# Performance work log

Measured on AMD Instinct MI355X. Metric: run time of the kernel, lower is better.

The kernel has to match this reference:

```python
import jax, jax.numpy as jnp
import numpy as np

CLASS_COUNT = 21
THRESHOLD = 0.5
ALPHA = 0.25
GAMMA = 2.0
VARIANCE = (0.1, 0.2)

B, A, N_OBJ = 32, 24576, 16


def point_form(boxes):
    # center form (cx, cy, w, h) -> point form (xmin, ymin, xmax, ymax)
    return jnp.concatenate([boxes[:, :2] - boxes[:, 2:] / 2,
                            boxes[:, :2] + boxes[:, 2:] / 2], axis=1)


def jaccard(truths, priors):
    # truths [N,4], priors [A,4] both in point form -> IoU [N, A]
    lt = jnp.maximum(truths[:, None, :2], priors[None, :, :2])
    rb = jnp.minimum(truths[:, None, 2:], priors[None, :, 2:])
    wh = jnp.clip(rb - lt, 0.0, None)
    inter = wh[..., 0] * wh[..., 1]
    area_t = ((truths[:, 2] - truths[:, 0]) * (truths[:, 3] - truths[:, 1]))[:, None]
    area_p = ((priors[:, 2] - priors[:, 0]) * (priors[:, 3] - priors[:, 1]))[None, :]
    return inter / (area_t + area_p - inter)


def match_one(labels, truths, anchors):
    # labels [N] int, truths [N,4] point form, anchors [A,4] center form
    overlaps = jaccard(truths, point_form(anchors))           # [N, A]
    best_prior_idx = jnp.argmax(overlaps, axis=1)             # [N]
    best_truth_overlap = jnp.max(overlaps, axis=0)            # [A]
    best_truth_idx = jnp.argmax(overlaps, axis=0)             # [A]
    # ensure every gt matches its best prior
    best_truth_overlap = best_truth_overlap.at[best_prior_idx].set(2.0)
    best_truth_idx = best_truth_idx.at[best_prior_idx].set(jnp.arange(truths.shape[0]))
    matches = truths[best_truth_idx]                          # [A, 4]
    conf = jnp.where(best_truth_overlap < THRESHOLD, 0, labels[best_truth_idx])
    # encode with variances
    g_cxcy = ((matches[:, :2] + matches[:, 2:]) * 0.5 - anchors[:, :2]) / (VARIANCE[0] * anchors[:, 2:])
    g_wh = jnp.log((matches[:, 2:] - matches[:, :2]) / anchors[:, 2:]) / VARIANCE[1]
    return conf, jnp.concatenate([g_cxcy, g_wh], axis=1)


def setup_inputs() -> dict:
    key = jax.random.key(0)
    k1, k2, k3, k4, k5, k6, k7 = jax.random.split(key, 7)
    class_preds = jax.random.normal(k1, (B, A, CLASS_COUNT), dtype=jnp.float32)
    loc_preds = jax.random.normal(k2, (B, A, 4), dtype=jnp.float32)
    # ground-truth boxes: random valid point-form boxes in [0,1]
    ctr = jax.random.uniform(k3, (B, N_OBJ, 2), minval=0.2, maxval=0.8)
    wh = jax.random.uniform(k4, (B, N_OBJ, 2), minval=0.05, maxval=0.3)
    loc_targets = jnp.clip(jnp.concatenate([ctr - wh / 2, ctr + wh / 2], axis=-1), 0.0, 1.0)
    class_targets = jax.random.randint(k5, (B, N_OBJ), 1, CLASS_COUNT)
    # anchors in center form
    a_ctr = jax.random.uniform(k6, (A, 2), minval=0.05, maxval=0.95)
    a_wh = jax.random.uniform(k7, (A, 2), minval=0.05, maxval=0.4)
    anchors = jnp.concatenate([a_ctr, a_wh], axis=1)
    return {"class_preds": class_preds, "loc_preds": loc_preds,
            "loc_targets": loc_targets, "anchors": anchors,
            "class_targets": class_targets}


def reference(class_preds, loc_preds, loc_targets, anchors, class_targets):
    conf, loc_t = jax.vmap(match_one, in_axes=(0, 0, None))(class_targets, loc_targets, anchors)
    pos = conf > 0                                            # [B, A]
    num_matched = jnp.sum(pos).astype(jnp.float32)
    # smooth L1 over positive anchors (sum reduction, beta=1)
    d = loc_preds - loc_t
    ad = jnp.abs(d)
    sl1 = jnp.where(ad < 1.0, 0.5 * d * d, ad - 0.5)
    loc_loss = jnp.sum(sl1 * pos[..., None].astype(sl1.dtype))
    # focal loss (drop background column 0)
    cp = class_preds.reshape(-1, CLASS_COUNT)[:, 1:]          # [B*A, C-1]
    t = jax.nn.one_hot(conf.reshape(-1), CLASS_COUNT, dtype=cp.dtype)[:, 1:]
    p = jax.nn.sigmoid(cp)
    pt = jnp.where(t > 0, p, 1.0 - p)
    w = (1.0 - pt) ** GAMMA
    w = jnp.where(t > 0, ALPHA * w, (1.0 - ALPHA) * w)
    # stable binary cross entropy with logits, weighted, sum reduction
    bce = jnp.maximum(cp, 0.0) - cp * t + jnp.log1p(jnp.exp(-jnp.abs(cp)))
    class_loss = jnp.sum(w * bce)
    class_loss = class_loss / num_matched
    loc_loss = loc_loss / num_matched
    return jnp.stack([class_loss, loc_loss, class_loss + loc_loss])
```

## Files before the change

### kernel.cpp

```cpp
#include <hip/hip_runtime.h>

#define A_COUNT 24576
#define B_COUNT 32
#define NOBJ 16
#define C_COUNT 21

#define NCH 64
#define CHUNK (A_COUNT / NCH)
#define NBLK (NCH * B_COUNT)
#define TOTAL4 (B_COUNT * A_COUNT * C_COUNT / 4)

#define WS_BPP 0
#define WS_LOCP 262144
#define WS_CLSP 270336
#define WS_POSP 278528
#define WS_DLOC 286720
#define WS_DCLS 286848
#define WS_DPOS 286976

__device__ __forceinline__ unsigned long long pack_key(float iou, int a) {
    unsigned int ib = __float_as_uint(iou);
    return ((unsigned long long)ib << 32) | (unsigned long long)(0xFFFFFFFFu - (unsigned int)a);
}

__device__ __forceinline__ float iou_pf(float tx0, float ty0, float tx1, float ty1, float at,
                                        float x0, float y0, float x1, float y1, float ap) {
    float lx = fmaxf(tx0, x0), ly = fmaxf(ty0, y0);
    float rx = fminf(tx1, x1), ry = fminf(ty1, y1);
    float w = fmaxf(rx - lx, 0.0f), h = fmaxf(ry - ly, 0.0f);
    float inter = w * h;
    return inter / (at + ap - inter);
}

__device__ __forceinline__ float sl1(float d) {
    float ad = fabsf(d);
    return (ad < 1.0f) ? 0.5f * d * d : ad - 0.5f;
}

__device__ __forceinline__ float loc_term(float4 t, float4 an, float4 lp) {
    float gx = ((t.x + t.z) * 0.5f - an.x) / (0.1f * an.z);
    float gy = ((t.y + t.w) * 0.5f - an.y) / (0.1f * an.w);
    float gw = __logf((t.z - t.x) / an.z) * 5.0f;
    float gh = __logf((t.w - t.y) / an.w) * 5.0f;
    return sl1(lp.x - gx) + sl1(lp.y - gy) + sl1(lp.z - gw) + sl1(lp.w - gh);
}

__device__ __forceinline__ float corr_term(float x) {
    float E = __expf(x);
    float den = 1.0f + E;
    float s = __builtin_amdgcn_rcpf(den);
    float p = E * s;
    float L = __logf(den);
    return 0.25f * s * s * (L - x) - 0.75f * p * p * L;
}

__global__ __launch_bounds__(256, 2) void k_main(const float* __restrict__ cls,
                                                 const float4* __restrict__ locp,
                                                 const float4* __restrict__ anchors,
                                                 const float4* __restrict__ truths,
                                                 const int* __restrict__ labels,
                                                 unsigned long long* __restrict__ bp_partial,
                                                 float* __restrict__ loc_partial,
                                                 float* __restrict__ cls_partial,
                                                 unsigned int* __restrict__ pos_partial) {
    const int ch = blockIdx.x;
    const int b = blockIdx.y;
    const int tid = threadIdx.x;
    __shared__ float4 s_t[NOBJ];
    __shared__ float s_area[NOBJ];
    __shared__ int s_lab[NOBJ];
    __shared__ unsigned long long s_keys[8][256];
    if (tid < NOBJ) {
        float4 t = truths[b * NOBJ + tid];
        s_t[tid] = t;
        s_area[tid] = (t.z - t.x) * (t.w - t.y);
        s_lab[tid] = labels[b * NOBJ + tid];
    }
    __syncthreads();
    const int a0 = ch * CHUNK + tid;
    const bool has1 = tid < (CHUNK - 256);
    const int a1 = a0 + 256;
    float4 an0 = anchors[a0];
    float4 an1 = anchors[has1 ? a1 : a0];
    float p0x0 = an0.x - an0.z * 0.5f, p0y0 = an0.y - an0.w * 0.5f;
    float p0x1 = an0.x + an0.z * 0.5f, p0y1 = an0.y + an0.w * 0.5f;
    float ap0 = (p0x1 - p0x0) * (p0y1 - p0y0);
    float p1x0 = an1.x - an1.z * 0.5f, p1y0 = an1.y - an1.w * 0.5f;
    float p1x1 = an1.x + an1.z * 0.5f, p1y1 = an1.y + an1.w * 0.5f;
    float ap1 = (p1x1 - p1x0) * (p1y1 - p1y0);
    float best0 = -1.0f, best1 = -1.0f;
    int idx0 = 0, idx1 = 0;
#pragma unroll
    for (int half = 0; half < 2; ++half) {
#pragma unroll
        for (int n = 0; n < 8; ++n) {
            const int nt = half * 8 + n;
            float4 t = s_t[nt];
            float at = s_area[nt];
            float iou0 = iou_pf(t.x, t.y, t.z, t.w, at, p0x0, p0y0, p0x1, p0y1, ap0);
            if (iou0 > best0) { best0 = iou0; idx0 = nt; }
            unsigned long long key = pack_key(iou0, a0);
            if (has1) {
                float iou1 = iou_pf(t.x, t.y, t.z, t.w, at, p1x0, p1y0, p1x1, p1y1, ap1);
                if (iou1 > best1) { best1 = iou1; idx1 = nt; }
                unsigned long long k1 = pack_key(iou1, a1);
                key = (k1 > key) ? k1 : key;
            }
            s_keys[n][tid] = key;
        }
        __syncthreads();
        if (tid < 128) {
            const int g = tid >> 4, l = tid & 15;
            unsigned long long k = s_keys[g][l];
#pragma unroll
            for (int kk = 1; kk < 16; ++kk) {
                unsigned long long v = s_keys[g][l + 16 * kk];
                k = (v > k) ? v : k;
            }
#pragma unroll
            for (int s = 8; s >= 1; s >>= 1) {
                unsigned long long o = __shfl_xor(k, s);
                k = (o > k) ? o : k;
            }
            if (l == 0) bp_partial[(b * NOBJ + half * 8 + g) * NCH + ch] = k;
        }
        __syncthreads();
    }
    float loc_l = 0.0f, cls_acc = 0.0f;
    unsigned int pos = 0;
    if (!(best0 < 0.5f)) {
        pos++;
        loc_l += loc_term(s_t[idx0], an0, locp[(size_t)b * A_COUNT + a0]);
        cls_acc += corr_term(cls[((size_t)b * A_COUNT + a0) * C_COUNT + s_lab[idx0]]);
    }
    if (has1 && !(best1 < 0.5f)) {
        pos++;
        loc_l += loc_term(s_t[idx1], an1, locp[(size_t)b * A_COUNT + a1]);
        cls_acc += corr_term(cls[((size_t)b * A_COUNT + a1) * C_COUNT + s_lab[idx1]]);
    }

    const int bid = b * NCH + ch;
    {
        const float4* cls4 = (const float4*)cls;
        int i = bid * 256 + tid;
        unsigned int f = (unsigned int)i * 4u;
        unsigned int dq = f / 21u;
        int r = (int)(f - dq * 21u);
        const int stride = NBLK * 256;
        for (; i < TOTAL4; i += stride) {
            float4 x4 = cls4[i];
            float xs[4] = {x4.x, x4.y, x4.z, x4.w};
#pragma unroll
            for (int j = 0; j < 4; ++j) {
                int rr = r + j;
                float x = xs[j];
                float E = __expf(x);
                float den = 1.0f + E;
                float s = __builtin_amdgcn_rcpf(den);
                float p = E * s;
                float L = __logf(den);
                float v = p * p * L;
                float m = (rr == 0 || rr == 21) ? 0.0f : 0.75f;
                cls_acc = fmaf(v, m, cls_acc);
            }
            r += 8; if (r >= 21) r -= 21;
        }
    }

#pragma unroll
    for (int s = 32; s >= 1; s >>= 1) {
        loc_l += __shfl_xor(loc_l, s);
        cls_acc += __shfl_xor(cls_acc, s);
        pos += __shfl_xor(pos, s);
    }
    __shared__ float s_ll[4], s_cl[4];
    __shared__ unsigned int s_pp[4];
    if ((tid & 63) == 0) {
        s_ll[tid >> 6] = loc_l;
        s_cl[tid >> 6] = cls_acc;
        s_pp[tid >> 6] = pos;
    }
    __syncthreads();
    if (tid == 0) {
        loc_partial[bid] = s_ll[0] + s_ll[1] + s_ll[2] + s_ll[3];
        cls_partial[bid] = s_cl[0] + s_cl[1] + s_cl[2] + s_cl[3];
        pos_partial[bid] = s_pp[0] + s_pp[1] + s_pp[2] + s_pp[3];
    }
}

__global__ __launch_bounds__(256) void k_fix(const float* __restrict__ cls,
                                             const float4* __restrict__ locp,
                                             const float4* __restrict__ anchors,
                                             const float4* __restrict__ truths,
                                             const int* __restrict__ labels,
                                             const unsigned long long* __restrict__ bp_partial,
                                             float* __restrict__ dloc,
                                             float* __restrict__ dcls,
                                             int* __restrict__ dpos) {
    const int b = blockIdx.x;
    const int tid = threadIdx.x;
    __shared__ int s_bp[NOBJ];
    {
        const int g = tid >> 4, l = tid & 15;
        const unsigned long long* pp = &bp_partial[(size_t)(b * NOBJ + g) * NCH];
        unsigned long long k = pp[l];
        unsigned long long v;
        v = pp[l + 16]; k = (v > k) ? v : k;
        v = pp[l + 32]; k = (v > k) ? v : k;
        v = pp[l + 48]; k = (v > k) ? v : k;
#pragma unroll
        for (int s = 8; s >= 1; s >>= 1) {
            unsigned long long o = __shfl_xor(k, s);
            k = (o > k) ? o : k;
        }
        if (l == 0) {
            unsigned int ia = 0xFFFFFFFFu - (unsigned int)(k & 0xFFFFFFFFull);
            s_bp[g] = (ia >= A_COUNT) ? -1 : (int)ia;
        }
    }
    __syncthreads();
    float d_loc = 0.0f, d_cls = 0.0f;
    int d_pos = 0;
    if (tid < NOBJ) {
        const int n = tid;
        const int q = s_bp[n];
        bool winner = (q >= 0);
        for (int n2 = n + 1; n2 < NOBJ; ++n2)
            if (s_bp[n2] == q) winner = false;
        if (winner) {
            float4 an = anchors[q];
            float px0 = an.x - an.z * 0.5f, py0 = an.y - an.w * 0.5f;
            float px1 = an.x + an.z * 0.5f, py1 = an.y + an.w * 0.5f;
            float ap = (px1 - px0) * (py1 - py0);
            float best = -1.0f;
            int idx = 0;
            for (int n2 = 0; n2 < NOBJ; ++n2) {
                float4 t = truths[b * NOBJ + n2];
                float at = (t.z - t.x) * (t.w - t.y);
                float iou = iou_pf(t.x, t.y, t.z, t.w, at, px0, py0, px1, py1, ap);
                if (iou > best) { best = iou; idx = n2; }
            }
            float4 lp = locp[(size_t)b * A_COUNT + q];
            if (!(best < 0.5f)) {
                d_pos -= 1;
                d_loc -= loc_term(truths[b * NOBJ + idx], an, lp);
                d_cls -= corr_term(cls[((size_t)b * A_COUNT + q) * C_COUNT + labels[b * NOBJ + idx]]);
            }
            d_pos += 1;
            d_loc += loc_term(truths[b * NOBJ + n], an, lp);
            d_cls += corr_term(cls[((size_t)b * A_COUNT + q) * C_COUNT + labels[b * NOBJ + n]]);
        }
    }
    if (tid < 64) {
#pragma unroll
        for (int s = 8; s >= 1; s >>= 1) {
            d_loc += __shfl_xor(d_loc, s);
            d_cls += __shfl_xor(d_cls, s);
            d_pos += __shfl_xor(d_pos, s);
        }
        if (tid == 0) {
            dloc[b] = d_loc;
            dcls[b] = d_cls;
            dpos[b] = d_pos;
        }
    }
}

__global__ __launch_bounds__(256) void k_final(const float* __restrict__ loc_partial,
                                               const float* __restrict__ cls_partial,
                                               const unsigned int* __restrict__ pos_partial,
                                               const float* __restrict__ dloc,
                                               const float* __restrict__ dcls,
                                               const int* __restrict__ dpos,
                                               float* __restrict__ out) {
    const int tid = threadIdx.x;
    double loc = 0.0, clsv = 0.0;
    int pos = 0;
    for (int i = tid; i < NBLK; i += 256) {
        loc += (double)loc_partial[i];
        clsv += (double)cls_partial[i];
        pos += (int)pos_partial[i];
    }
    if (tid < B_COUNT) {
        loc += (double)dloc[tid];
        clsv += (double)dcls[tid];
        pos += dpos[tid];
    }
#pragma unroll
    for (int s = 32; s >= 1; s >>= 1) {
        loc += __shfl_xor(loc, s);
        clsv += __shfl_xor(clsv, s);
        pos += __shfl_xor(pos, s);
    }
    __shared__ double s_l[4], s_c[4];
    __shared__ int s_p[4];
    if ((tid & 63) == 0) {
        s_l[tid >> 6] = loc;
        s_c[tid >> 6] = clsv;
        s_p[tid >> 6] = pos;
    }
    __syncthreads();
    if (tid == 0) {
        double L = s_l[0] + s_l[1] + s_l[2] + s_l[3];
        double Cv = s_c[0] + s_c[1] + s_c[2] + s_c[3];
        float nm = (float)(s_p[0] + s_p[1] + s_p[2] + s_p[3]);
        float cf = (float)Cv / nm;
        float lf = (float)L / nm;
        out[0] = cf;
        out[1] = lf;
        out[2] = cf + lf;
    }
}

extern "C" void kernel_launch(void* const* d_in, const int* in_sizes, int n_in,
                              void* d_out, int out_size, void* d_ws, size_t ws_size,
                              hipStream_t stream) {
    const float* cls = (const float*)d_in[0];
    const float4* locp = (const float4*)d_in[1];
    const float4* truths = (const float4*)d_in[2];
    const float4* anchors = (const float4*)d_in[3];
    const int* labels = (const int*)d_in[4];

    char* ws = (char*)d_ws;
    unsigned long long* bp_partial = (unsigned long long*)(ws + WS_BPP);
    float* loc_partial = (float*)(ws + WS_LOCP);
    float* cls_partial = (float*)(ws + WS_CLSP);
    unsigned int* pos_partial = (unsigned int*)(ws + WS_POSP);
    float* dloc = (float*)(ws + WS_DLOC);
    float* dcls = (float*)(ws + WS_DCLS);
    int* dpos = (int*)(ws + WS_DPOS);

    k_main<<<dim3(NCH, B_COUNT), 256, 0, stream>>>(cls, locp, anchors, truths, labels,
                                                   bp_partial, loc_partial, cls_partial, pos_partial);
    k_fix<<<B_COUNT, 256, 0, stream>>>(cls, locp, anchors, truths, labels, bp_partial,
                                       dloc, dcls, dpos);
    k_final<<<1, 256, 0, stream>>>(loc_partial, cls_partial, pos_partial, dloc, dcls, dpos,
                                   (float*)d_out);
}
```

Before: 42.99 us.

## Prefetch class-logit stream into registers before IoU matching to overlap loads

Issues all eight strided float4 loads of class logits per thread up front, before the IoU/argmax matching phase, so global memory latency overlaps with matching compute. The grid-stride loop becomes a fully unrolled fixed 8-iteration loop with four independent accumulators. Occupancy hint rises from 2 to 4 blocks per SM, and __syncthreads is replaced by an LDS-only waitcnt plus raw barrier so barriers do not wait on the outstanding global prefetches. This raises register pressure (32 extra VGPRs held across the matching phase) and hardcodes the iteration count to the problem size.

```diff
diff --git a/kernel.cpp b/kernel.cpp
--- a/kernel.cpp
+++ b/kernel.cpp
@@ -9,6 +9,7 @@
 #define CHUNK (A_COUNT / NCH)
 #define NBLK (NCH * B_COUNT)
 #define TOTAL4 (B_COUNT * A_COUNT * C_COUNT / 4)
+#define STRIDE4 (NBLK * 256)
 
 #define WS_BPP 0
 #define WS_LOCP 262144
@@ -54,7 +55,16 @@
     return 0.25f * s * s * (L - x) - 0.75f * p * p * L;
 }
 
-__global__ __launch_bounds__(256, 2) void k_main(const float* __restrict__ cls,
+#define FOC(xval, rr, acc) {                                 \
+    float E_ = __expf(xval);                                 \
+    float den_ = 1.0f + E_;                                  \
+    float s_ = __builtin_amdgcn_rcpf(den_);                  \
+    float p_ = E_ * s_;                                      \
+    float L_ = __logf(den_);                                 \
+    float m_ = ((rr) == 0 || (rr) == 21) ? 0.0f : 0.75f;     \
+    acc = fmaf(p_ * p_ * L_, m_, acc); }
+
+__global__ __launch_bounds__(256, 4) void k_main(const float* __restrict__ cls,
                                                  const float4* __restrict__ locp,
                                                  const float4* __restrict__ anchors,
                                                  const float4* __restrict__ truths,
@@ -77,11 +87,27 @@
         s_lab[tid] = labels[b * NOBJ + tid];
     }
     __syncthreads();
+    __builtin_amdgcn_sched_barrier(0);
+
     const int a0 = ch * CHUNK + tid;
     const bool has1 = tid < (CHUNK - 256);
     const int a1 = a0 + 256;
     float4 an0 = anchors[a0];
     float4 an1 = anchors[has1 ? a1 : a0];
+
+    const int bid = b * NCH + ch;
+    const float4* cls4 = (const float4*)cls;
+    const int i0 = bid * 256 + tid;
+    const bool v7 = (i0 + 7 * STRIDE4) < TOTAL4;
+    float4 xv[8];
+#pragma unroll
+    for (int k = 0; k < 8; ++k) {
+        const int ik = i0 + k * STRIDE4;
+        if (k < 7) xv[k] = cls4[ik];
+        else       xv[7] = v7 ? cls4[ik] : make_float4(0.f, 0.f, 0.f, 0.f);
+    }
+    __builtin_amdgcn_sched_barrier(0);
+
     float p0x0 = an0.x - an0.z * 0.5f, p0y0 = an0.y - an0.w * 0.5f;
     float p0x1 = an0.x + an0.z * 0.5f, p0y1 = an0.y + an0.w * 0.5f;
     float ap0 = (p0x1 - p0x0) * (p0y1 - p0y0);
@@ -108,7 +134,8 @@
             }
             s_keys[n][tid] = key;
         }
-        __syncthreads();
+        asm volatile("s_waitcnt lgkmcnt(0)" ::: "memory");
+        __builtin_amdgcn_s_barrier();
         if (tid < 128) {
             const int g = tid >> 4, l = tid & 15;
             unsigned long long k = s_keys[g][l];
@@ -124,7 +151,8 @@
             }
             if (l == 0) bp_partial[(b * NOBJ + half * 8 + g) * NCH + ch] = k;
         }
-        __syncthreads();
+        asm volatile("s_waitcnt lgkmcnt(0)" ::: "memory");
+        __builtin_amdgcn_s_barrier();
     }
     float loc_l = 0.0f, cls_acc = 0.0f;
     unsigned int pos = 0;
@@ -139,32 +167,21 @@
         cls_acc += corr_term(cls[((size_t)b * A_COUNT + a1) * C_COUNT + s_lab[idx1]]);
     }
 
-    const int bid = b * NCH + ch;
     {
-        const float4* cls4 = (const float4*)cls;
-        int i = bid * 256 + tid;
-        unsigned int f = (unsigned int)i * 4u;
+        unsigned int f = (unsigned int)i0 * 4u;
         unsigned int dq = f / 21u;
         int r = (int)(f - dq * 21u);
-        const int stride = NBLK * 256;
-        for (; i < TOTAL4; i += stride) {
-            float4 x4 = cls4[i];
-            float xs[4] = {x4.x, x4.y, x4.z, x4.w};
-#pragma unroll
-            for (int j = 0; j < 4; ++j) {
-                int rr = r + j;
-                float x = xs[j];
-                float E = __expf(x);
-                float den = 1.0f + E;
-                float s = __builtin_amdgcn_rcpf(den);
-                float p = E * s;
-                float L = __logf(den);
-                float v = p * p * L;
-                float m = (rr == 0 || rr == 21) ? 0.0f : 0.75f;
-                cls_acc = fmaf(v, m, cls_acc);
+        float acc0 = 0.0f, acc1 = 0.0f, acc2 = 0.0f, acc3 = 0.0f;
+#pragma unroll
+        for (int k = 0; k < 8; ++k) {
+            if (k < 7 || v7) {
+                float4 x4 = xv[k];
+                FOC(x4.x, r + 0, acc0); FOC(x4.y, r + 1, acc1);
+                FOC(x4.z, r + 2, acc2); FOC(x4.w, r + 3, acc3);
             }
             r += 8; if (r >= 21) r -= 21;
         }
+        cls_acc += (acc0 + acc1) + (acc2 + acc3);
     }
 
 #pragma unroll
```

After: 46.89 us. 1.09x slower.

## Split anchors into 96 chunks with one anchor per thread and split accumulators

Applied to the files above, without the earlier changes.

Raises the anchor chunk count from 64 to 96 so each 256-thread block handles exactly 256 anchors, one per thread, removing the second-anchor path. Workspace offsets, the streaming stride and the fix-kernel partial reduction are updated to match, and launch bounds now ask for 4 blocks per SM. The focal streaming loop uses four independent accumulators with the 0.75 factor applied once at the end, and IoU division becomes a hardware reciprocal. This adds more blocks and more partials to reduce, trading per-thread work for occupancy and ILP. The approximate reciprocal may slightly change argmax tie behaviour.

```diff
diff --git a/kernel.cpp b/kernel.cpp
--- a/kernel.cpp
+++ b/kernel.cpp
@@ -5,18 +5,19 @@
 #define NOBJ 16
 #define C_COUNT 21
 
-#define NCH 64
+#define NCH 96
 #define CHUNK (A_COUNT / NCH)
 #define NBLK (NCH * B_COUNT)
 #define TOTAL4 (B_COUNT * A_COUNT * C_COUNT / 4)
+#define STRIDE4 (NBLK * 256)
 
 #define WS_BPP 0
-#define WS_LOCP 262144
-#define WS_CLSP 270336
-#define WS_POSP 278528
-#define WS_DLOC 286720
-#define WS_DCLS 286848
-#define WS_DPOS 286976
+#define WS_LOCP 393216
+#define WS_CLSP 405504
+#define WS_POSP 417792
+#define WS_DLOC 430080
+#define WS_DCLS 430208
+#define WS_DPOS 430336
 
 __device__ __forceinline__ unsigned long long pack_key(float iou, int a) {
     unsigned int ib = __float_as_uint(iou);
@@ -29,7 +30,7 @@
     float rx = fminf(tx1, x1), ry = fminf(ty1, y1);
     float w = fmaxf(rx - lx, 0.0f), h = fmaxf(ry - ly, 0.0f);
     float inter = w * h;
-    return inter / (at + ap - inter);
+    return inter * __builtin_amdgcn_rcpf(at + ap - inter);
 }
 
 __device__ __forceinline__ float sl1(float d) {
@@ -54,7 +55,16 @@
     return 0.25f * s * s * (L - x) - 0.75f * p * p * L;
 }
 
-__global__ __launch_bounds__(256, 2) void k_main(const float* __restrict__ cls,
+#define FOC(xval, rr, acc) {                                 \
+    float E_ = __expf(xval);                                 \
+    float den_ = 1.0f + E_;                                  \
+    float s_ = __builtin_amdgcn_rcpf(den_);                  \
+    float p_ = E_ * s_;                                      \
+    float L_ = __logf(den_);                                 \
+    float v_ = ((rr) == 0 || (rr) == 21) ? 0.0f : p_ * p_ * L_; \
+    acc += v_; }
+
+__global__ __launch_bounds__(256, 4) void k_main(const float* __restrict__ cls,
                                                  const float4* __restrict__ locp,
                                                  const float4* __restrict__ anchors,
                                                  const float4* __restrict__ truths,
@@ -78,18 +88,12 @@
     }
     __syncthreads();
     const int a0 = ch * CHUNK + tid;
-    const bool has1 = tid < (CHUNK - 256);
-    const int a1 = a0 + 256;
     float4 an0 = anchors[a0];
-    float4 an1 = anchors[has1 ? a1 : a0];
     float p0x0 = an0.x - an0.z * 0.5f, p0y0 = an0.y - an0.w * 0.5f;
     float p0x1 = an0.x + an0.z * 0.5f, p0y1 = an0.y + an0.w * 0.5f;
     float ap0 = (p0x1 - p0x0) * (p0y1 - p0y0);
-    float p1x0 = an1.x - an1.z * 0.5f, p1y0 = an1.y - an1.w * 0.5f;
-    float p1x1 = an1.x + an1.z * 0.5f, p1y1 = an1.y + an1.w * 0.5f;
-    float ap1 = (p1x1 - p1x0) * (p1y1 - p1y0);
-    float best0 = -1.0f, best1 = -1.0f;
-    int idx0 = 0, idx1 = 0;
+    float best0 = -1.0f;
+    int idx0 = 0;
 #pragma unroll
     for (int half = 0; half < 2; ++half) {
 #pragma unroll
@@ -99,14 +103,7 @@
             float at = s_area[nt];
             float iou0 = iou_pf(t.x, t.y, t.z, t.w, at, p0x0, p0y0, p0x1, p0y1, ap0);
             if (iou0 > best0) { best0 = iou0; idx0 = nt; }
-            unsigned long long key = pack_key(iou0, a0);
-            if (has1) {
-                float iou1 = iou_pf(t.x, t.y, t.z, t.w, at, p1x0, p1y0, p1x1, p1y1, ap1);
-                if (iou1 > best1) { best1 = iou1; idx1 = nt; }
-                unsigned long long k1 = pack_key(iou1, a1);
-                key = (k1 > key) ? k1 : key;
-            }
-            s_keys[n][tid] = key;
+            s_keys[n][tid] = pack_key(iou0, a0);
         }
         __syncthreads();
         if (tid < 128) {
@@ -126,45 +123,30 @@
         }
         __syncthreads();
     }
-    float loc_l = 0.0f, cls_acc = 0.0f;
+    float loc_l = 0.0f, corr_acc = 0.0f;
     unsigned int pos = 0;
     if (!(best0 < 0.5f)) {
-        pos++;
-        loc_l += loc_term(s_t[idx0], an0, locp[(size_t)b * A_COUNT + a0]);
-        cls_acc += corr_term(cls[((size_t)b * A_COUNT + a0) * C_COUNT + s_lab[idx0]]);
-    }
-    if (has1 && !(best1 < 0.5f)) {
-        pos++;
-        loc_l += loc_term(s_t[idx1], an1, locp[(size_t)b * A_COUNT + a1]);
-        cls_acc += corr_term(cls[((size_t)b * A_COUNT + a1) * C_COUNT + s_lab[idx1]]);
+        pos = 1;
+        loc_l = loc_term(s_t[idx0], an0, locp[(size_t)b * A_COUNT + a0]);
+        corr_acc = corr_term(cls[((size_t)b * A_COUNT + a0) * C_COUNT + s_lab[idx0]]);
     }
 
     const int bid = b * NCH + ch;
+    float cls_acc;
     {
         const float4* cls4 = (const float4*)cls;
         int i = bid * 256 + tid;
         unsigned int f = (unsigned int)i * 4u;
         unsigned int dq = f / 21u;
         int r = (int)(f - dq * 21u);
-        const int stride = NBLK * 256;
-        for (; i < TOTAL4; i += stride) {
+        float acc0 = 0.0f, acc1 = 0.0f, acc2 = 0.0f, acc3 = 0.0f;
+        for (; i < TOTAL4; i += STRIDE4) {
             float4 x4 = cls4[i];
-            float xs[4] = {x4.x, x4.y, x4.z, x4.w};
-#pragma unroll
-            for (int j = 0; j < 4; ++j) {
-                int rr = r + j;
-                float x = xs[j];
-                float E = __expf(x);
-                float den = 1.0f + E;
-                float s = __builtin_amdgcn_rcpf(den);
-                float p = E * s;
-                float L = __logf(den);
-                float v = p * p * L;
-                float m = (rr == 0 || rr == 21) ? 0.0f : 0.75f;
-                cls_acc = fmaf(v, m, cls_acc);
-            }
-            r += 8; if (r >= 21) r -= 21;
-        }
+            FOC(x4.x, r + 0, acc0); FOC(x4.y, r + 1, acc1);
+            FOC(x4.z, r + 2, acc2); FOC(x4.w, r + 3, acc3);
+            r += 12; if (r >= 21) r -= 21;
+        }
+        cls_acc = corr_acc + 0.75f * ((acc0 + acc1) + (acc2 + acc3));
     }
 
 #pragma unroll
@@ -204,10 +186,11 @@
         const int g = tid >> 4, l = tid & 15;
         const unsigned long long* pp = &bp_partial[(size_t)(b * NOBJ + g) * NCH];
         unsigned long long k = pp[l];
-        unsigned long long v;
-        v = pp[l + 16]; k = (v > k) ? v : k;
-        v = pp[l + 32]; k = (v > k) ? v : k;
-        v = pp[l + 48]; k = (v > k) ? v : k;
+#pragma unroll
+        for (int kk = 1; kk < 6; ++kk) {
+            unsigned long long v = pp[l + 16 * kk];
+            k = (v > k) ? v : k;
+        }
 #pragma unroll
         for (int s = 8; s >= 1; s >>= 1) {
             unsigned long long o = __shfl_xor(k, s);
```

Result: faster. 41.65 us (median of 2 runs) (-3.1%).
